# Kernel optimization log

Hardware: AMD Instinct MI355X
Metric: run time of the kernel (lower is better)

## Reference

```python
import jax, jax.numpy as jnp
import numpy as np

HEAD_DIM = 128  # dim // num_heads; RoPE rot_dim and softmax scale
ROPE_THETA = 10000.0


def rope_rotate(x, rot_dim):
    # lucidrains RotaryEmbedding.rotate_queries_or_keys: rotate first rot_dim
    # channels of last axis with interleaved-pair rotation; pass rest through.
    T = x.shape[-2]
    inv_freq = 1.0 / (ROPE_THETA ** (jnp.arange(0, rot_dim, 2, dtype=jnp.float32) / rot_dim))
    freqs = jnp.arange(T, dtype=jnp.float32)[:, None] * inv_freq[None, :]  # [T, rot_dim//2]
    freqs = jnp.repeat(freqs, 2, axis=-1)  # [T, rot_dim] interleaved (f0,f0,f1,f1,...)
    cos, sin = jnp.cos(freqs), jnp.sin(freqs)
    xr, x_pass = x[..., :rot_dim], x[..., rot_dim:]
    x1, x2 = xr[..., 0::2], xr[..., 1::2]
    rot = jnp.stack([-x2, x1], axis=-1).reshape(xr.shape)  # rotate_half
    xr = xr * cos + rot * sin
    return jnp.concatenate([xr, x_pass], axis=-1)


def setup_inputs() -> dict:
    key = jax.random.key(0)
    ks = jax.random.split(key, 9)
    B, T, D = 2, 2048, 2048
    w = lambda k, shape: jax.random.normal(k, shape, dtype=jnp.float32) * 0.02
    return {
        "latent_space": jax.random.normal(ks[0], (B, T, D), dtype=jnp.float32),
        "Wq": w(ks[1], (D, D)), "bq": w(ks[2], (D,)),
        "Wk": w(ks[3], (D, D)), "bk": w(ks[4], (D,)),
        "Wv": w(ks[5], (D, D)), "bv": w(ks[6], (D,)),
        "Wfc": w(ks[7], (D, D)), "bfc": w(ks[8], (D,)),
    }


def reference(latent_space, Wq, bq, Wk, bk, Wv, bv, Wfc, bfc):
    # Projections (nn.Linear: x @ W.T + b)
    Q = latent_space @ Wq.T + bq
    K = latent_space @ Wk.T + bk
    V = latent_space @ Wv.T + bv
    # Fused RoPE on first HEAD_DIM channels (module never splits heads)
    Q = rope_rotate(Q, HEAD_DIM)
    K = rope_rotate(K, HEAD_DIM)
    # Full-hidden-dim QK^T: [B,T,T]
    qk = jnp.einsum('btd,bsd->bts', Q, K)
    T = qk.shape[-1]
    causal = jnp.triu(jnp.ones((T, T), dtype=bool), 1)
    A = jnp.where(causal, -jnp.inf, qk)
    # PartialSoftmax with temp=1, h_t=None: state = A/sqrt(head_dim);
    # out = exp(state)/sum(exp(state)) * 2
    state = A / jnp.sqrt(jnp.float32(HEAD_DIM))
    x_exp = jnp.exp(state)
    A = x_exp / jnp.sum(x_exp, axis=-1, keepdims=True) * 2.0
    out = jnp.einsum('bts,bsd->btd', A, V) @ Wfc.T + bfc
    return out
```

## Files before the change

kernel.cpp:

```cpp
#include <hip/hip_runtime.h>
#include <hip/hip_bf16.h>
#include <math.h>

using bf16 = __hip_bfloat16;
typedef __attribute__((ext_vector_type(8))) __bf16 bf16x8;
typedef __attribute__((ext_vector_type(4))) float f32x4;

#define SBAR() asm volatile("s_barrier" ::: "memory")
#define WAITVM(n) asm volatile("s_waitcnt vmcnt(" #n ")" ::: "memory")
#define LGKM0() { asm volatile("s_waitcnt lgkmcnt(0)" ::: "memory"); __builtin_amdgcn_sched_barrier(0); }
#define DSR(dst, a, o) asm volatile("ds_read_b128 %0, %1 offset:" o : "=v"(dst) : "v"(a))

static __device__ __forceinline__ void gload16(const bf16* g, bf16* l) {
  __builtin_amdgcn_global_load_lds((const __attribute__((address_space(1))) void*)g,
                                   (__attribute__((address_space(3))) void*)l, 16, 0, 0);
}

struct GP {
  const bf16* A[6]; const bf16* B[6]; char* C[6];
  const float* bias[6];
  int K[6], flags[6], ktOff[6];
};
struct CvtP { const float* s[5]; bf16* d[5]; int n4[5]; };

__global__ __launch_bounds__(256) void cvt_f32_bf16(CvtP p) {
  const int y = blockIdx.y;
  const int i = blockIdx.x * 256 + threadIdx.x;
  if (i >= p.n4[y]) return;
  const float4 v = reinterpret_cast<const float4*>(p.s[y])[i];
  union { bf16 h[4]; short4 s4; } u;
  u.h[0] = __float2bfloat16(v.x);
  u.h[1] = __float2bfloat16(v.y);
  u.h[2] = __float2bfloat16(v.z);
  u.h[3] = __float2bfloat16(v.w);
  *reinterpret_cast<short4*>(p.d[y] + 4 * (size_t)i) = u.s4;
}

__global__ __launch_bounds__(512, 1) void gemm8p(GP P, int lda, int ldb, int ldc) {
  const int z = blockIdx.z;
  const int fl = P.flags[z];
  if ((fl & 1) && blockIdx.x > blockIdx.y) return;
  const int by = (fl & 8) ? ((int)gridDim.y - 1 - (int)blockIdx.y) : (int)blockIdx.y;
  const int rowBase = by * 256;
  const int colBase = (int)blockIdx.x * 256;
  int kEnd = P.K[z];
  if (fl & 8) {
    const int lim = rowBase + 256 - P.ktOff[z];
    kEnd = kEnd < lim ? kEnd : lim;
    if (kEnd <= 0) return;
  }
  const int NT = kEnd >> 6;

  const int tid  = threadIdx.x;
  const int lane = tid & 63;
  const int wid  = tid >> 6;
  const int wm = wid >> 2;
  const int wn = wid & 3;

  __shared__ alignas(16) bf16 ls[2][4][8192];

  f32x4 acc[8][4] = {};

  const int r0  = tid >> 2;
  const int sw8 = ((tid & 3) ^ ((r0 >> 1) & 3)) * 8;
  const bf16* gA = P.A[z] + (size_t)(rowBase + r0) * lda + sw8;
  const bf16* gB = P.B[z] + (size_t)(colBase + r0) * ldb + sw8;

  const uint lsbase = (uint)(size_t)(__attribute__((address_space(3))) void*)&ls[0][0][0];
  const int lr = lane >> 4, lc = lane & 15;
  uint aB[8], bB[4];
#pragma unroll
  for (int mi = 0; mi < 8; ++mi) {
    const int row = wm * 128 + mi * 16 + lc;
    aB[mi] = lsbase + (uint)(row * 64 + (lr ^ ((row >> 1) & 3)) * 16);
  }
#pragma unroll
  for (int ni = 0; ni < 4; ++ni) {
    const int row = wn * 64 + ni * 16 + lc;
    bB[ni] = lsbase + 32768u + (uint)(row * 64 + (lr ^ ((row >> 1) & 3)) * 16);
  }

#define STG(t, h) { bf16* d = &ls[(t) & 1][h][0]; \
    if ((h) < 2) { const int ko = (t) * 64 + (h) * 32; \
      gload16(gA + ko, &d[tid * 8]); \
      gload16(gA + (size_t)128 * lda + ko, &d[4096 + tid * 8]); \
    } else { const int ko = (t) * 64 + ((h) - 2) * 32; \
      gload16(gB + ko, &d[tid * 8]); \
      gload16(gB + (size_t)128 * ldb + ko, &d[4096 + tid * 8]); } }

  STG(0, 0); STG(0, 2); STG(0, 1); STG(0, 3);
  WAITVM(0);
  SBAR();

  for (int t = 0; t < NT; ++t) {
    const uint dsel = (uint)(t & 1) << 16;
    uint ao[8], bo[4];
#pragma unroll
    for (int i = 0; i < 8; ++i) ao[i] = aB[i] + dsel;
#pragma unroll
    for (int i = 0; i < 4; ++i) bo[i] = bB[i] + dsel;
    const bool more = (t + 1 < NT);
    bf16x8 a0[4], a1[4], b0[4], b1[4];

#pragma unroll
    for (int i = 0; i < 4; ++i) DSR(a0[i], ao[i], "0");
#pragma unroll
    for (int i = 0; i < 4; ++i) DSR(b0[i], bo[i], "0");
    if (more) STG(t + 1, 0);
    SBAR();
    LGKM0();
    __builtin_amdgcn_s_setprio(1);
#pragma unroll
    for (int m = 0; m < 4; ++m)
#pragma unroll
      for (int n = 0; n < 4; ++n)
        acc[m][n] = __builtin_amdgcn_mfma_f32_16x16x32_bf16(a0[m], b0[n], acc[m][n], 0, 0, 0);
    __builtin_amdgcn_s_setprio(0);
    SBAR();

#pragma unroll
    for (int i = 0; i < 4; ++i) DSR(a1[i], ao[4 + i], "0");
    if (more) STG(t + 1, 2);
    if (t + 1 == NT) { WAITVM(0); } else { WAITVM(4); }
    SBAR();
    LGKM0();
    __builtin_amdgcn_s_setprio(1);
#pragma unroll
    for (int m = 0; m < 4; ++m)
#pragma unroll
      for (int n = 0; n < 4; ++n)
        acc[4 + m][n] = __builtin_amdgcn_mfma_f32_16x16x32_bf16(a1[m], b0[n], acc[4 + m][n], 0, 0, 0);
    __builtin_amdgcn_s_setprio(0);
    SBAR();

#pragma unroll
    for (int i = 0; i < 4; ++i) DSR(a0[i], ao[i], "16384");
#pragma unroll
    for (int i = 0; i < 4; ++i) DSR(b1[i], bo[i], "16384");
    if (more) STG(t + 1, 1);
    SBAR();
    LGKM0();
    __builtin_amdgcn_s_setprio(1);
#pragma unroll
    for (int m = 0; m < 4; ++m)
#pragma unroll
      for (int n = 0; n < 4; ++n)
        acc[m][n] = __builtin_amdgcn_mfma_f32_16x16x32_bf16(a0[m], b1[n], acc[m][n], 0, 0, 0);
    __builtin_amdgcn_s_setprio(0);
    SBAR();

#pragma unroll
    for (int i = 0; i < 4; ++i) DSR(a1[i], ao[4 + i], "16384");
    if (more) STG(t + 1, 3);
    WAITVM(4);
    SBAR();
    LGKM0();
    __builtin_amdgcn_s_setprio(1);
#pragma unroll
    for (int m = 0; m < 4; ++m)
#pragma unroll
      for (int n = 0; n < 4; ++n)
        acc[4 + m][n] = __builtin_amdgcn_mfma_f32_16x16x32_bf16(a1[m], b1[n], acc[4 + m][n], 0, 0, 0);
    __builtin_amdgcn_s_setprio(0);
    SBAR();
  }
#undef STG

  const float* bias = P.bias[z];
  char* C = P.C[z];
#pragma unroll
  for (int m = 0; m < 8; ++m) {
    const int row0 = rowBase + wm * 128 + m * 16 + lr * 4;
#pragma unroll
    for (int n = 0; n < 4; ++n) {
      const int col = colBase + wn * 64 + n * 16 + lc;
      const float bcol = (bias && !(fl & 2)) ? bias[col] : 0.f;
#pragma unroll
      for (int j = 0; j < 4; ++j) {
        float v = acc[m][n][j] + bcol;
        if (fl & 2) v += bias[row0 + j];
        const long idx = (long)(row0 + j) * ldc + col;
        if (fl & 4) reinterpret_cast<float*>(C)[idx] = v;
        else        reinterpret_cast<bf16*>(C)[idx] = __float2bfloat16(v);
      }
    }
  }
}

__global__ __launch_bounds__(256) void rope_bf16(bf16* __restrict__ X) {
  const int idx = blockIdx.x * 256 + threadIdx.x;
  const int row = idx >> 6;
  const int i   = idx & 63;
  const int t   = row & 2047;
  const float ang = (float)t * exp2f((float)i * -0.20762050593046f);
  float sn, cs;
  sincosf(ang, &sn, &cs);
  bf16* p = X + ((long)row << 11) + 2 * i;
  const float x1 = __bfloat162float(p[0]);
  const float x2 = __bfloat162float(p[1]);
  p[0] = __float2bfloat16(x1 * cs - x2 * sn);
  p[1] = __float2bfloat16(x2 * cs + x1 * sn);
}

__global__ __launch_bounds__(256) void softmax_causal(
    const float* __restrict__ S0, const float* __restrict__ S1,
    const float* __restrict__ S2, const float* __restrict__ S3,
    bf16* __restrict__ A0, bf16* __restrict__ A1) {
  const int t = blockIdx.x;
  const int b = blockIdx.y;
  const float* ra = (b ? S2 : S0) + (long)t * 2048;
  const float* rb = (b ? S3 : S1) + (long)t * 2048;
  bf16* orow = (b ? A1 : A0) + (long)t * 4096;
  const int L = t + 1;
  __shared__ float e[2048];
  __shared__ float red[4];
  const float scale = 0.0883883476483184f;
  const int lane = threadIdx.x & 63, wd = threadIdx.x >> 6;

  float mx = -INFINITY;
  for (int s = threadIdx.x; s < L; s += 256) {
    const float v = (ra[s] + rb[s]) * scale;
    e[s] = v;
    mx = fmaxf(mx, v);
  }
#pragma unroll
  for (int off = 1; off < 64; off <<= 1) mx = fmaxf(mx, __shfl_xor(mx, off));
  if (lane == 0) red[wd] = mx;
  __syncthreads();
  mx = fmaxf(fmaxf(red[0], red[1]), fmaxf(red[2], red[3]));
  __syncthreads();

  float sum = 0.f;
  for (int s = threadIdx.x; s < L; s += 256) {
    const float v = expf(e[s] - mx);
    e[s] = v;
    sum += v;
  }
#pragma unroll
  for (int off = 1; off < 64; off <<= 1) sum += __shfl_xor(sum, off);
  if (lane == 0) red[wd] = sum;
  __syncthreads();
  sum = red[0] + red[1] + red[2] + red[3];
  const float f = 2.f / sum;
  for (int s = threadIdx.x; s < 2048; s += 256) {
    const float v = (s < L) ? e[s] * f : 0.f;
    orow[s] = __float2bfloat16(v);
  }
}

__global__ __launch_bounds__(256) void pv_reduce(
    const float* __restrict__ p0a, const float* __restrict__ p0b,
    const float* __restrict__ p1, bf16* __restrict__ O) {
  const long i4 = (long)blockIdx.x * 256 + threadIdx.x;
  const long g = i4 * 4;
  const int b = (int)(g >> 22);
  const long rem = g & ((1L << 22) - 1);
  const int r = (int)(rem >> 11);
  const float* p0 = b ? p0b : p0a;
  float4 v = *reinterpret_cast<const float4*>(p0 + rem);
  if (r >= 1024) {
    const float4 w = *reinterpret_cast<const float4*>(
        p1 + (long)b * (1024 * 2048) + (rem - (1L << 21)));
    v.x += w.x; v.y += w.y; v.z += w.z; v.w += w.w;
  }
  union { bf16 h[4]; short4 s; } u;
  u.h[0] = __float2bfloat16(v.x);
  u.h[1] = __float2bfloat16(v.y);
  u.h[2] = __float2bfloat16(v.z);
  u.h[3] = __float2bfloat16(v.w);
  *reinterpret_cast<short4*>(O + g) = u.s;
}

__global__ __launch_bounds__(256) void fc_reduce(
    const float* __restrict__ pa, const float* __restrict__ pb,
    const float* __restrict__ bias, float* __restrict__ out) {
  const long i4 = (long)blockIdx.x * 256 + threadIdx.x;
  const long g = i4 * 4;
  const int col = (int)(g & 2047);
  const float4 a = reinterpret_cast<const float4*>(pa)[i4];
  const float4 b4 = reinterpret_cast<const float4*>(pb)[i4];
  const float4 bv = *reinterpret_cast<const float4*>(bias + col);
  float4 o;
  o.x = a.x + b4.x + bv.x;
  o.y = a.y + b4.y + bv.y;
  o.z = a.z + b4.z + bv.z;
  o.w = a.w + b4.w + bv.w;
  reinterpret_cast<float4*>(out)[i4] = o;
}

extern "C" void kernel_launch(void* const* d_in, const int* in_sizes, int n_in,
                              void* d_out, int out_size, void* d_ws, size_t ws_size,
                              hipStream_t stream) {
  (void)in_sizes; (void)n_in; (void)out_size; (void)ws_size;
  const float* lat = (const float*)d_in[0];
  const float* Wq  = (const float*)d_in[1];
  const float* bq  = (const float*)d_in[2];
  const float* Wk  = (const float*)d_in[3];
  const float* bk  = (const float*)d_in[4];
  const float* Wv  = (const float*)d_in[5];
  const float* bv  = (const float*)d_in[6];
  const float* Wfc = (const float*)d_in[7];
  const float* bfc = (const float*)d_in[8];
  float* out = (float*)d_out;

  constexpr long T = 2048, D = 2048, MT = 4096;
  constexpr long TTB = T * T * 4;
  char* w = (char*)d_ws;
  bf16* latb = (bf16*)w;  w += MT * D * 2;
  bf16* wqb  = (bf16*)w;  w += D * D * 2;
  bf16* wkb  = (bf16*)w;  w += D * D * 2;
  bf16* wvb  = (bf16*)w;  w += D * D * 2;
  bf16* wfb  = (bf16*)w;  w += D * D * 2;
  bf16* Qb   = (bf16*)w;  w += MT * D * 2;
  bf16* Kb   = (bf16*)w;  w += MT * D * 2;
  bf16* VTb  = (bf16*)w;  w += MT * D * 2;
  float* S0  = (float*)w; w += TTB;
  float* S1  = (float*)w; w += TTB;
  float* P1w = (float*)w; w += TTB;
  float* S2  = (float*)d_out;
  float* S3  = (float*)((char*)d_out + TTB);
  bf16* A0   = (bf16*)S0;
  bf16* A1   = (bf16*)S3;
  float* P0a = S1;
  float* P0b = S2;
  bf16* Ob   = latb;
  float* Pf0 = (float*)Qb;
  float* Pf1 = S0;

  CvtP cp;
  cp.s[0] = lat; cp.d[0] = latb; cp.n4[0] = (int)(MT * D / 4);
  cp.s[1] = Wq;  cp.d[1] = wqb;  cp.n4[1] = (int)(D * D / 4);
  cp.s[2] = Wk;  cp.d[2] = wkb;  cp.n4[2] = (int)(D * D / 4);
  cp.s[3] = Wv;  cp.d[3] = wvb;  cp.n4[3] = (int)(D * D / 4);
  cp.s[4] = Wfc; cp.d[4] = wfb;  cp.n4[4] = (int)(D * D / 4);
  cvt_f32_bf16<<<dim3(8192, 5), 256, 0, stream>>>(cp);

  {
    GP P = {};
    P.A[0] = latb; P.B[0] = wqb; P.C[0] = (char*)Qb; P.bias[0] = bq; P.K[0] = 2048;
    P.A[1] = latb; P.B[1] = wkb; P.C[1] = (char*)Kb; P.bias[1] = bk; P.K[1] = 2048;
    gemm8p<<<dim3(8, 16, 2), 512, 0, stream>>>(P, 2048, 2048, 2048);
  }

  rope_bf16<<<2048, 256, 0, stream>>>(Qb);

  {
    GP P = {};
    for (int b = 0; b < 2; ++b) {
      P.A[b] = wvb; P.B[b] = latb + (long)b * T * D;
      P.C[b] = (char*)(VTb + (long)b * T * D);
      P.bias[b] = bv; P.K[b] = 2048; P.flags[b] = 2;
    }
    char* sc[4] = {(char*)S0, (char*)S1, (char*)S2, (char*)S3};
    for (int zz = 0; zz < 4; ++zz) {
      const int b = zz >> 1, kh = zz & 1;
      P.A[2 + zz] = Qb + (long)b * T * D + kh * 1024;
      P.B[2 + zz] = Kb + (long)b * T * D + kh * 1024;
      P.C[2 + zz] = sc[zz];
      P.K[2 + zz] = 1024; P.flags[2 + zz] = 1 | 4;
    }
    gemm8p<<<dim3(8, 8, 6), 512, 0, stream>>>(P, 2048, 2048, 2048);
  }

  softmax_causal<<<dim3(2048, 2), 256, 0, stream>>>(S0, S1, S2, S3, A0, A1);

  {
    GP P = {};
    for (int z = 0; z < 4; ++z) {
      const int b = z >> 1, kh = z & 1;
      P.A[z] = (b ? A1 : A0) + kh * 1024;
      P.B[z] = VTb + (long)b * T * D + kh * 1024;
      P.C[z] = kh ? ((char*)P1w + (long)b * 1024 * 2048 * 4 - (long)1024 * 2048 * 4)
                  : (char*)(b ? P0b : P0a);
      P.K[z] = 1024; P.flags[z] = 8 | 4; P.ktOff[z] = kh * 1024;
    }
    gemm8p<<<dim3(8, 8, 4), 512, 0, stream>>>(P, 4096, 2048, 2048);
  }

  pv_reduce<<<8192, 256, 0, stream>>>(P0a, P0b, P1w, Ob);

  {
    GP P = {};
    for (int kh = 0; kh < 2; ++kh) {
      P.A[kh] = Ob + kh * 1024;
      P.B[kh] = wfb + kh * 1024;
      P.C[kh] = (char*)(kh ? Pf1 : Pf0);
      P.K[kh] = 1024; P.flags[kh] = 4;
    }
    gemm8p<<<dim3(8, 16, 2), 512, 0, stream>>>(P, 2048, 2048, 2048);
  }

  fc_reduce<<<8192, 256, 0, stream>>>(Pf0, Pf1, bfc, out);
}
```

Measured before the change: 311.5 us.

## Drop trailing per-phase barriers in GEMM loop and un-split the FC GEMM

```diff
diff --git a/kernel.cpp b/kernel.cpp
--- a/kernel.cpp
+++ b/kernel.cpp
@@ -116,7 +116,6 @@
       for (int n = 0; n < 4; ++n)
         acc[m][n] = __builtin_amdgcn_mfma_f32_16x16x32_bf16(a0[m], b0[n], acc[m][n], 0, 0, 0);
     __builtin_amdgcn_s_setprio(0);
-    SBAR();
 
 #pragma unroll
     for (int i = 0; i < 4; ++i) DSR(a1[i], ao[4 + i], "0");
@@ -131,7 +130,6 @@
       for (int n = 0; n < 4; ++n)
         acc[4 + m][n] = __builtin_amdgcn_mfma_f32_16x16x32_bf16(a1[m], b0[n], acc[4 + m][n], 0, 0, 0);
     __builtin_amdgcn_s_setprio(0);
-    SBAR();
 
 #pragma unroll
     for (int i = 0; i < 4; ++i) DSR(a0[i], ao[i], "16384");
@@ -147,7 +145,6 @@
       for (int n = 0; n < 4; ++n)
         acc[m][n] = __builtin_amdgcn_mfma_f32_16x16x32_bf16(a0[m], b1[n], acc[m][n], 0, 0, 0);
     __builtin_amdgcn_s_setprio(0);
-    SBAR();
 
 #pragma unroll
     for (int i = 0; i < 4; ++i) DSR(a1[i], ao[4 + i], "16384");
@@ -162,7 +159,6 @@
       for (int n = 0; n < 4; ++n)
         acc[4 + m][n] = __builtin_amdgcn_mfma_f32_16x16x32_bf16(a1[m], b1[n], acc[4 + m][n], 0, 0, 0);
     __builtin_amdgcn_s_setprio(0);
-    SBAR();
   }
 #undef STG
 
@@ -269,23 +265,6 @@
   u.h[2] = __float2bfloat16(v.z);
   u.h[3] = __float2bfloat16(v.w);
   *reinterpret_cast<short4*>(O + g) = u.s;
-}
-
-__global__ __launch_bounds__(256) void fc_reduce(
-    const float* __restrict__ pa, const float* __restrict__ pb,
-    const float* __restrict__ bias, float* __restrict__ out) {
-  const long i4 = (long)blockIdx.x * 256 + threadIdx.x;
-  const long g = i4 * 4;
-  const int col = (int)(g & 2047);
-  const float4 a = reinterpret_cast<const float4*>(pa)[i4];
-  const float4 b4 = reinterpret_cast<const float4*>(pb)[i4];
-  const float4 bv = *reinterpret_cast<const float4*>(bias + col);
-  float4 o;
-  o.x = a.x + b4.x + bv.x;
-  o.y = a.y + b4.y + bv.y;
-  o.z = a.z + b4.z + bv.z;
-  o.w = a.w + b4.w + bv.w;
-  reinterpret_cast<float4*>(out)[i4] = o;
 }
 
 extern "C" void kernel_launch(void* const* d_in, const int* in_sizes, int n_in,
@@ -324,8 +303,6 @@
   float* P0a = S1;
   float* P0b = S2;
   bf16* Ob   = latb;
-  float* Pf0 = (float*)Qb;
-  float* Pf1 = S0;
 
   CvtP cp;
   cp.s[0] = lat; cp.d[0] = latb; cp.n4[0] = (int)(MT * D / 4);
@@ -381,14 +358,8 @@
 
   {
     GP P = {};
-    for (int kh = 0; kh < 2; ++kh) {
-      P.A[kh] = Ob + kh * 1024;
-      P.B[kh] = wfb + kh * 1024;
-      P.C[kh] = (char*)(kh ? Pf1 : Pf0);
-      P.K[kh] = 1024; P.flags[kh] = 4;
-    }
-    gemm8p<<<dim3(8, 16, 2), 512, 0, stream>>>(P, 2048, 2048, 2048);
-  }
-
-  fc_reduce<<<8192, 256, 0, stream>>>(Pf0, Pf1, bfc, out);
-}
+    P.A[0] = Ob; P.B[0] = wfb; P.C[0] = (char*)out;
+    P.bias[0] = bfc; P.K[0] = 2048; P.flags[0] = 4;
+    gemm8p<<<dim3(8, 16, 1), 512, 0, stream>>>(P, 2048, 2048, 2048);
+  }
+}
```

Measured after the change: 298.6 us. 1.04x faster.

## Fuse RoPE into projection GEMM epilogue, drop trailing barriers, trim softmax zero-fill

Applied to the files above, without the earlier changes.

```diff
diff --git a/kernel.cpp b/kernel.cpp
--- a/kernel.cpp
+++ b/kernel.cpp
@@ -116,7 +116,6 @@
       for (int n = 0; n < 4; ++n)
         acc[m][n] = __builtin_amdgcn_mfma_f32_16x16x32_bf16(a0[m], b0[n], acc[m][n], 0, 0, 0);
     __builtin_amdgcn_s_setprio(0);
-    SBAR();
 
 #pragma unroll
     for (int i = 0; i < 4; ++i) DSR(a1[i], ao[4 + i], "0");
@@ -131,7 +130,6 @@
       for (int n = 0; n < 4; ++n)
         acc[4 + m][n] = __builtin_amdgcn_mfma_f32_16x16x32_bf16(a1[m], b0[n], acc[4 + m][n], 0, 0, 0);
     __builtin_amdgcn_s_setprio(0);
-    SBAR();
 
 #pragma unroll
     for (int i = 0; i < 4; ++i) DSR(a0[i], ao[i], "16384");
@@ -147,7 +145,6 @@
       for (int n = 0; n < 4; ++n)
         acc[m][n] = __builtin_amdgcn_mfma_f32_16x16x32_bf16(a0[m], b1[n], acc[m][n], 0, 0, 0);
     __builtin_amdgcn_s_setprio(0);
-    SBAR();
 
 #pragma unroll
     for (int i = 0; i < 4; ++i) DSR(a1[i], ao[4 + i], "16384");
@@ -162,7 +159,6 @@
       for (int n = 0; n < 4; ++n)
         acc[4 + m][n] = __builtin_amdgcn_mfma_f32_16x16x32_bf16(a1[m], b1[n], acc[4 + m][n], 0, 0, 0);
     __builtin_amdgcn_s_setprio(0);
-    SBAR();
   }
 #undef STG
 
@@ -179,27 +175,20 @@
       for (int j = 0; j < 4; ++j) {
         float v = acc[m][n][j] + bcol;
         if (fl & 2) v += bias[row0 + j];
+        if ((fl & 16) && col < 128) {
+          const float prt = __shfl_xor(v, 1);
+          const int tpos = (row0 + j) & 2047;
+          const float ang = (float)tpos * exp2f((float)(col >> 1) * -0.20762050593046f);
+          float sn, cs;
+          sincosf(ang, &sn, &cs);
+          v = (col & 1) ? (v * cs + prt * sn) : (v * cs - prt * sn);
+        }
         const long idx = (long)(row0 + j) * ldc + col;
         if (fl & 4) reinterpret_cast<float*>(C)[idx] = v;
         else        reinterpret_cast<bf16*>(C)[idx] = __float2bfloat16(v);
       }
     }
   }
-}
-
-__global__ __launch_bounds__(256) void rope_bf16(bf16* __restrict__ X) {
-  const int idx = blockIdx.x * 256 + threadIdx.x;
-  const int row = idx >> 6;
-  const int i   = idx & 63;
-  const int t   = row & 2047;
-  const float ang = (float)t * exp2f((float)i * -0.20762050593046f);
-  float sn, cs;
-  sincosf(ang, &sn, &cs);
-  bf16* p = X + ((long)row << 11) + 2 * i;
-  const float x1 = __bfloat162float(p[0]);
-  const float x2 = __bfloat162float(p[1]);
-  p[0] = __float2bfloat16(x1 * cs - x2 * sn);
-  p[1] = __float2bfloat16(x2 * cs + x1 * sn);
 }
 
 __global__ __launch_bounds__(256) void softmax_causal(
@@ -212,6 +201,7 @@
   const float* rb = (b ? S3 : S1) + (long)t * 2048;
   bf16* orow = (b ? A1 : A0) + (long)t * 4096;
   const int L = t + 1;
+  const int zEnd = ((t >> 8) + 1) << 8;
   __shared__ float e[2048];
   __shared__ float red[4];
   const float scale = 0.0883883476483184f;
@@ -242,7 +232,7 @@
   __syncthreads();
   sum = red[0] + red[1] + red[2] + red[3];
   const float f = 2.f / sum;
-  for (int s = threadIdx.x; s < 2048; s += 256) {
+  for (int s = threadIdx.x; s < zEnd; s += 256) {
     const float v = (s < L) ? e[s] * f : 0.f;
     orow[s] = __float2bfloat16(v);
   }
@@ -337,12 +327,12 @@
 
   {
     GP P = {};
-    P.A[0] = latb; P.B[0] = wqb; P.C[0] = (char*)Qb; P.bias[0] = bq; P.K[0] = 2048;
-    P.A[1] = latb; P.B[1] = wkb; P.C[1] = (char*)Kb; P.bias[1] = bk; P.K[1] = 2048;
+    P.A[0] = latb; P.B[0] = wqb; P.C[0] = (char*)Qb; P.bias[0] = bq;
+    P.K[0] = 2048; P.flags[0] = 16;
+    P.A[1] = latb; P.B[1] = wkb; P.C[1] = (char*)Kb; P.bias[1] = bk;
+    P.K[1] = 2048; P.flags[1] = 16;
     gemm8p<<<dim3(8, 16, 2), 512, 0, stream>>>(P, 2048, 2048, 2048);
   }
-
-  rope_bf16<<<2048, 256, 0, stream>>>(Qb);
 
   {
     GP P = {};
```

New measurement: 367.9 us. 18.1% more time.
